# Kernel tuning notes

Hardware: AMD Instinct MI355X
Metric: run time of the kernel (lower is better)

The kernel has to match this reference:

```python
import jax, jax.numpy as jnp
import numpy as np
from jax import lax


def setup_inputs() -> dict:
    key = jax.random.key(0)
    ks = jax.random.split(key, 8)
    N, L, I, H = 256, 512, 512, 1024
    s_i = 1.0 / np.sqrt(H)
    x = jax.random.normal(ks[0], (N, L, I), dtype=jnp.float32)
    h = jnp.zeros((N, H), dtype=jnp.float32)
    # GRUCell params (torch layout: weight_ih [3H, I], weight_hh [3H, H], gate order r,z,n)
    W_ih = jax.random.uniform(ks[1], (3 * H, I), dtype=jnp.float32, minval=-s_i, maxval=s_i)
    b_ih = jax.random.uniform(ks[2], (3 * H,), dtype=jnp.float32, minval=-s_i, maxval=s_i)
    W_hh = jax.random.uniform(ks[3], (3 * H, H), dtype=jnp.float32, minval=-s_i, maxval=s_i)
    b_hh = jax.random.uniform(ks[4], (3 * H,), dtype=jnp.float32, minval=-s_i, maxval=s_i)
    # fc_out: Linear(H, I)
    W_out = jax.random.uniform(ks[5], (I, H), dtype=jnp.float32, minval=-s_i, maxval=s_i)
    b_out = jax.random.uniform(ks[6], (I,), dtype=jnp.float32, minval=-s_i, maxval=s_i)
    return {"x": x, "h": h, "W_ih": W_ih, "b_ih": b_ih, "W_hh": W_hh, "b_hh": b_hh,
            "W_out": W_out, "b_out": b_out}


def reference(x, h, W_ih, b_ih, W_hh, b_hh, W_out, b_out):
    # Many-to-one GRU: scan GRUCell over time, linear head on final hidden state.
    def step(h, xt):
        gi = xt @ W_ih.T + b_ih          # [N, 3H]
        gh = h @ W_hh.T + b_hh           # [N, 3H]
        i_r, i_z, i_n = jnp.split(gi, 3, axis=-1)
        h_r, h_z, h_n = jnp.split(gh, 3, axis=-1)
        r = jax.nn.sigmoid(i_r + h_r)
        z = jax.nn.sigmoid(i_z + h_z)
        n = jnp.tanh(i_n + r * h_n)
        h_new = (1.0 - z) * n + z * h
        return h_new, None

    xs = jnp.swapaxes(x, 0, 1)           # [L, N, I] for scan over time
    h_final, _ = lax.scan(step, h, xs)
    y = h_final @ W_out.T + b_out        # [N, I]
    return (y, h_final)
```

## Files before the change

kernel.cpp:

```cpp
#include <hip/hip_runtime.h>


typedef unsigned short u16;
typedef unsigned int   u32;
typedef __attribute__((ext_vector_type(4))) float f32x4;
typedef __attribute__((ext_vector_type(8))) short s16x8;

constexpr int NB   = 256;
constexpr int LSEQ = 512;
constexpr int ISZ  = 512;
constexpr int HSZ  = 1024;

constexpr int TILE_U16  = 48 * 1536;
constexpr int TILEBYTES = TILE_U16 * 2;
constexpr int LDS_TOTAL = TILEBYTES;

__device__ __forceinline__ u16 bf16_trunc(float f) {
    union { float f; unsigned u; } v; v.f = f;
    return (u16)(v.u >> 16);
}
__device__ __forceinline__ float bf16_up(u16 h) {
    union { float f; unsigned u; } v; v.u = ((unsigned)h) << 16;
    return v.f;
}
__device__ __forceinline__ u16 bf16_rtn(float f) {
    union { float f; unsigned u; } v; v.f = f;
    u32 u = v.u;
    u += 0x7FFFu + ((u >> 16) & 1u);
    return (u16)(u >> 16);
}

#define GLL16(g, l) __builtin_amdgcn_global_load_lds(                          \
    (const __attribute__((address_space(1))) u32*)(g),                         \
    (__attribute__((address_space(3))) u32*)(l), 16, 0, 0)

#define MFMA2(acc, a, b_h, b_l)                                              \
    acc = __builtin_amdgcn_mfma_f32_16x16x32_bf16(a, b_h, acc, 0, 0, 0);     \
    acc = __builtin_amdgcn_mfma_f32_16x16x32_bf16(a, b_l, acc, 0, 0, 0);

__global__ __launch_bounds__(256) void prep_kernel(
    const float* __restrict__ W_ih, const float* __restrict__ W_hh,
    const float* __restrict__ b_ih, const float* __restrict__ b_hh,
    const float* __restrict__ W_out,
    u16* __restrict__ Bhi, u16* __restrict__ Blo,
    float* __restrict__ Wt, float4* __restrict__ bias4)
{
    int idx = blockIdx.x * 256 + threadIdx.x;
    if (idx < 64 * TILE_U16) {
        int c   = idx / TILE_U16;
        int r1  = idx % TILE_U16;
        int kb  = r1 / 1536;
        int r2  = r1 % 1536;
        int p   = r2 / 512;
        int r3  = r2 % 512;
        int kg  = r3 >> 7;
        int col = (r3 >> 3) & 15;
        int e   = r3 & 7;
        int kloc = kg * 8 + e;
        int gcol = c * 16 + col;
        float w;
        if (kb < 16) w = W_ih[(p * HSZ + gcol) * ISZ + kb * 32 + kloc];
        else         w = W_hh[(p * HSZ + gcol) * HSZ + (kb - 16) * 32 + kloc];
        u16 hi = bf16_trunc(w);
        Bhi[idx] = hi;
        Blo[idx] = bf16_trunc(w - bf16_up(hi));
    }
    if (idx < HSZ * ISZ) {
        int i = idx % ISZ, k = idx / ISZ;
        Wt[idx] = W_out[i * HSZ + k];
    }
    if (idx < HSZ) {
        bias4[idx] = make_float4(b_ih[idx] + b_hh[idx],
                                 b_ih[HSZ + idx] + b_hh[HSZ + idx],
                                 b_ih[2 * HSZ + idx],
                                 b_hh[2 * HSZ + idx]);
    }
}

__global__ __launch_bounds__(256) void init_kernel(
    const float* __restrict__ x, const float* __restrict__ h_in,
    u16* __restrict__ xb0, float* __restrict__ hf0, u16* __restrict__ hb0)
{
    int idx = blockIdx.x * 256 + threadIdx.x;
    {
        int n = idx >> 9, k = idx & (ISZ - 1);
        xb0[idx] = bf16_rtn(x[(size_t)n * (LSEQ * ISZ) + k]);
    }
    #pragma unroll
    for (int q = 0; q < 2; ++q) {
        int e = idx * 2 + q;
        float v = h_in[e];
        hf0[e] = v;
        hb0[e] = bf16_rtn(v);
    }
}

__global__ __launch_bounds__(768, 1) void gru_step(
    const float* __restrict__ x, int t,
    const u16* __restrict__ Bhi, const u16* __restrict__ Blo,
    const float4* __restrict__ bias4,
    const u16* __restrict__ xb, u16* __restrict__ xb_n,
    const float* __restrict__ hf, const u16* __restrict__ hb,
    float* __restrict__ hf_n, u16* __restrict__ hb_n)
{
    extern __shared__ char lds[];

    const int tid  = threadIdx.x;
    const int lane = tid & 63;
    const int wv   = tid >> 6;
    const int raw  = blockIdx.x;
    const int c    = ((raw & 7) << 3) | ((raw >> 3) & 7);
    const int m    = raw >> 6;
    const int lr   = lane & 15;
    const int kg   = lane >> 4;
    const int fro  = kg * 256 + lr * 16;

    const char* tsrc = (const char*)Bhi + (size_t)c * TILEBYTES;

    #pragma unroll
    for (int i = 0; i < 12; ++i) {
        int seg = i * 12 + wv;
        GLL16(tsrc + seg * 1024 + lane * 16, lds + seg * 1024);
    }

    if (t + 1 < LSEQ && tid < 512) {
        int e = raw * 512 + tid;
        int n = e >> 9, k = e & (ISZ - 1);
        xb_n[e] = bf16_rtn(x[(size_t)n * (LSEQ * ISZ) + (size_t)(t + 1) * ISZ + k]);
    }

    __syncthreads();

    f32x4 acc[4][4];
    #pragma unroll
    for (int rt = 0; rt < 4; ++rt)
        #pragma unroll
        for (int s = 0; s < 4; ++s) acc[rt][s] = (f32x4){0.f, 0.f, 0.f, 0.f};

    const u16* blo = Blo + (size_t)c * TILE_U16;
    const bool isx = (wv < 4);

    #pragma unroll
    for (int j = 0; j < 4; ++j) {
        const int kbg = wv * 4 + j;
        const char* lp = lds + kbg * 3072 + fro;
        s16x8 bh0 = *(const s16x8*)lp;
        s16x8 bh1 = *(const s16x8*)(lp + 1024);
        s16x8 bh2 = *(const s16x8*)(lp + 2048);
        const u16* gp = blo + kbg * 1536 + kg * 128 + lr * 8;
        s16x8 bl0 = *(const s16x8*)gp;
        s16x8 bl1 = *(const s16x8*)(gp + 512);
        s16x8 bl2 = *(const s16x8*)(gp + 1024);

        #pragma unroll
        for (int rt = 0; rt < 4; ++rt) {
            const int row = m * 64 + rt * 16 + lr;
            s16x8 a;
            if (isx) a = *(const s16x8*)(xb + row * ISZ + kbg * 32 + kg * 8);
            else     a = *(const s16x8*)(hb + row * HSZ + (kbg - 16) * 32 + kg * 8);
            MFMA2(acc[rt][0], a, bh0, bl0)
            MFMA2(acc[rt][1], a, bh1, bl1)
            if (isx) { MFMA2(acc[rt][2], a, bh2, bl2) }
            else     { MFMA2(acc[rt][3], a, bh2, bl2) }
        }
    }

    float* scrf = (float*)lds;
    __syncthreads();
    if (wv >= 6) {
        float* sp = scrf + (wv - 6) * 4096 + lane * 4;
        #pragma unroll
        for (int rt = 0; rt < 4; ++rt)
            #pragma unroll
            for (int s = 0; s < 4; ++s)
                *(f32x4*)(sp + (rt * 4 + s) * 256) = acc[rt][s];
    }
    __syncthreads();
    if (wv < 6) {
        const float* sp = scrf + wv * 4096 + lane * 4;
        #pragma unroll
        for (int rt = 0; rt < 4; ++rt)
            #pragma unroll
            for (int s = 0; s < 4; ++s)
                acc[rt][s] += *(const f32x4*)(sp + (rt * 4 + s) * 256);
    }
    if (wv >= 3 && wv < 6) {
        float* sp = scrf + (wv + 3) * 4096 + lane * 4;
        #pragma unroll
        for (int rt = 0; rt < 4; ++rt)
            #pragma unroll
            for (int s = 0; s < 4; ++s)
                *(f32x4*)(sp + (rt * 4 + s) * 256) = acc[rt][s];
    }
    __syncthreads();
    if (wv < 3) {
        const float* sp = scrf + (wv + 6) * 4096 + lane * 4;
        float* wp = scrf + wv * 4096 + lane * 4;
        #pragma unroll
        for (int rt = 0; rt < 4; ++rt)
            #pragma unroll
            for (int s = 0; s < 4; ++s) {
                acc[rt][s] += *(const f32x4*)(sp + (rt * 4 + s) * 256);
                *(f32x4*)(wp + (rt * 4 + s) * 256) = acc[rt][s];
            }
    }
    __syncthreads();

    if (wv < 4) {
        const int rt = wv;
        f32x4 sr = {0,0,0,0}, sz = sr, sx = sr, sh = sr;
        #pragma unroll
        for (int sl = 0; sl < 3; ++sl) {
            const float* sp = scrf + sl * 4096 + lane * 4;
            sr += *(const f32x4*)(sp + (rt * 4 + 0) * 256);
            sz += *(const f32x4*)(sp + (rt * 4 + 1) * 256);
            sx += *(const f32x4*)(sp + (rt * 4 + 2) * 256);
            sh += *(const f32x4*)(sp + (rt * 4 + 3) * 256);
        }
        const int j = c * 16 + lr;
        const float4 b4 = bias4[j];
        #pragma unroll
        for (int i = 0; i < 4; ++i) {
            const int row = m * 64 + rt * 16 + kg * 4 + i;
            float rr  = 1.f / (1.f + __expf(-(sr[i] + b4.x)));
            float zz  = 1.f / (1.f + __expf(-(sz[i] + b4.y)));
            float pre = (sx[i] + b4.z) + rr * (sh[i] + b4.w);
            float e2  = __expf(2.f * pre);
            float ng  = 1.f - 2.f / (e2 + 1.f);
            float ho  = hf[row * HSZ + j];
            float hn  = (1.f - zz) * ng + zz * ho;
            hf_n[row * HSZ + j] = hn;
            hb_n[row * HSZ + j] = bf16_rtn(hn);
        }
    }
}

__global__ __launch_bounds__(256) void head_kernel(
    const float* __restrict__ hfin, const float* __restrict__ Wt,
    const float* __restrict__ b_out, float* __restrict__ out)
{
    __shared__ float hrow[HSZ];
    const int n = blockIdx.x;
    const int tid = threadIdx.x;
    for (int k = tid; k < HSZ; k += 256) {
        float v = hfin[n * HSZ + k];
        hrow[k] = v;
        out[NB * ISZ + n * HSZ + k] = v;
    }
    __syncthreads();
    for (int j = tid; j < ISZ; j += 256) {
        float acc = b_out[j];
        #pragma unroll 8
        for (int k = 0; k < HSZ; ++k)
            acc = fmaf(hrow[k], Wt[k * ISZ + j], acc);
        out[n * ISZ + j] = acc;
    }
}

extern "C" void kernel_launch(void* const* d_in, const int* in_sizes, int n_in,
                              void* d_out, int out_size, void* d_ws, size_t ws_size,
                              hipStream_t stream) {
    (void)in_sizes; (void)n_in; (void)out_size; (void)ws_size;
    const float* x     = (const float*)d_in[0];
    const float* h_in  = (const float*)d_in[1];
    const float* W_ih  = (const float*)d_in[2];
    const float* b_ih  = (const float*)d_in[3];
    const float* W_hh  = (const float*)d_in[4];
    const float* b_hh  = (const float*)d_in[5];
    const float* W_out = (const float*)d_in[6];
    const float* b_out = (const float*)d_in[7];
    float* out = (float*)d_out;

    char* ws = (char*)d_ws;
    size_t o = 0;
    u16*    Bhi   = (u16*)(ws + o);    o += (size_t)64 * TILEBYTES;
    u16*    Blo   = (u16*)(ws + o);    o += (size_t)64 * TILEBYTES;
    float*  Wt    = (float*)(ws + o);  o += (size_t)HSZ * ISZ * 4;
    float4* bias4 = (float4*)(ws + o); o += (size_t)HSZ * 16;
    float* hf[2]; u16 *hb[2], *xb[2];
    for (int b = 0; b < 2; ++b) { hf[b] = (float*)(ws + o); o += (size_t)NB * HSZ * 4; }
    for (int b = 0; b < 2; ++b) { hb[b] = (u16*)(ws + o);   o += (size_t)NB * HSZ * 2; }
    for (int b = 0; b < 2; ++b) { xb[b] = (u16*)(ws + o);   o += (size_t)NB * ISZ * 2; }

    prep_kernel<<<(64 * TILE_U16) / 256, 256, 0, stream>>>(
        W_ih, W_hh, b_ih, b_hh, W_out, Bhi, Blo, Wt, bias4);
    init_kernel<<<(NB * ISZ) / 256, 256, 0, stream>>>(
        x, h_in, xb[0], hf[0], hb[0]);

    for (int t = 0; t < LSEQ; ++t) {
        const int cur = t & 1, nxt = cur ^ 1;
        gru_step<<<256, 768, LDS_TOTAL, stream>>>(
            x, t, Bhi, Blo, bias4,
            xb[cur], xb[nxt],
            hf[cur], hb[cur],
            hf[nxt], hb[nxt]);
    }
    head_kernel<<<NB, 256, 0, stream>>>(hf[0], Wt, b_out, out);
}
```

Before: 6.747 ms.

## Replace per-timestep launches with persistent cooperative kernel and global atomic barriers

Turns the 512 per-step kernel launches into one cooperative persistent kernel with 256 blocks. Steps are synchronised through per-step atomic counters in global memory. Only the W_hh hi tile stays resident in LDS and the W_hh lo fragments are held in registers across steps. The input projection for step t+1 is computed right after each step, straight from fp32 x, so it overlaps the wait for the next barrier. This removes launch overhead and the repeated weight-tile reloads, at the cost of relaxed-atomic barrier correctness risk and higher register pressure with 512 threads and 2 blocks per CU.

```diff
diff --git a/kernel.cpp b/kernel.cpp
--- a/kernel.cpp
+++ b/kernel.cpp
@@ -1,8 +1,10 @@
 #include <hip/hip_runtime.h>
+#include <hip/hip_cooperative_groups.h>
 
 
 typedef unsigned short u16;
 typedef unsigned int   u32;
+typedef unsigned long long u64;
 typedef __attribute__((ext_vector_type(4))) float f32x4;
 typedef __attribute__((ext_vector_type(8))) short s16x8;
 
@@ -13,20 +15,18 @@
 
 constexpr int TILE_U16  = 48 * 1536;
 constexpr int TILEBYTES = TILE_U16 * 2;
-constexpr int LDS_TOTAL = TILEBYTES;
+constexpr int BH_LDS    = 96 * 1024;
+constexpr int LDS_TOTAL = BH_LDS + 32768;
 
 __device__ __forceinline__ u16 bf16_trunc(float f) {
-    union { float f; unsigned u; } v; v.f = f;
-    return (u16)(v.u >> 16);
+    union { float f; u32 u; } v; v.f = f; return (u16)(v.u >> 16);
 }
 __device__ __forceinline__ float bf16_up(u16 h) {
-    union { float f; unsigned u; } v; v.u = ((unsigned)h) << 16;
-    return v.f;
+    union { float f; u32 u; } v; v.u = ((u32)h) << 16; return v.f;
 }
 __device__ __forceinline__ u16 bf16_rtn(float f) {
-    union { float f; unsigned u; } v; v.f = f;
-    u32 u = v.u;
-    u += 0x7FFFu + ((u >> 16) & 1u);
+    union { float f; u32 u; } v; v.f = f;
+    u32 u = v.u; u += 0x7FFFu + ((u >> 16) & 1u);
     return (u16)(u >> 16);
 }
 
@@ -34,9 +34,7 @@
     (const __attribute__((address_space(1))) u32*)(g),                         \
     (__attribute__((address_space(3))) u32*)(l), 16, 0, 0)
 
-#define MFMA2(acc, a, b_h, b_l)                                              \
-    acc = __builtin_amdgcn_mfma_f32_16x16x32_bf16(a, b_h, acc, 0, 0, 0);     \
-    acc = __builtin_amdgcn_mfma_f32_16x16x32_bf16(a, b_l, acc, 0, 0, 0);
+#define MF(a, b, c) __builtin_amdgcn_mfma_f32_16x16x32_bf16(a, b, c, 0, 0, 0)
 
 __global__ __launch_bounds__(256) void prep_kernel(
     const float* __restrict__ W_ih, const float* __restrict__ W_hh,
@@ -78,58 +76,58 @@
 }
 
 __global__ __launch_bounds__(256) void init_kernel(
-    const float* __restrict__ x, const float* __restrict__ h_in,
-    u16* __restrict__ xb0, float* __restrict__ hf0, u16* __restrict__ hb0)
+    const float* __restrict__ h_in,
+    float* __restrict__ hf, u16* __restrict__ hb0, u32* __restrict__ bar)
 {
     int idx = blockIdx.x * 256 + threadIdx.x;
-    {
-        int n = idx >> 9, k = idx & (ISZ - 1);
-        xb0[idx] = bf16_rtn(x[(size_t)n * (LSEQ * ISZ) + k]);
-    }
-    #pragma unroll
-    for (int q = 0; q < 2; ++q) {
-        int e = idx * 2 + q;
-        float v = h_in[e];
-        hf0[e] = v;
-        hb0[e] = bf16_rtn(v);
-    }
-}
-
-__global__ __launch_bounds__(768, 1) void gru_step(
-    const float* __restrict__ x, int t,
+    float v = h_in[idx];
+    hf[idx]  = v;
+    hb0[idx] = bf16_rtn(v);
+    if (idx < LSEQ) bar[idx] = 0;
+}
+
+__global__ __launch_bounds__(512, 2) void gru_persistent(
+    const float* __restrict__ x,
     const u16* __restrict__ Bhi, const u16* __restrict__ Blo,
     const float4* __restrict__ bias4,
-    const u16* __restrict__ xb, u16* __restrict__ xb_n,
-    const float* __restrict__ hf, const u16* __restrict__ hb,
-    float* __restrict__ hf_n, u16* __restrict__ hb_n)
+    float* __restrict__ hf, u16* __restrict__ hb0, u16* __restrict__ hb1,
+    u32* __restrict__ bar)
 {
     extern __shared__ char lds[];
+    float* scr = (float*)(lds + BH_LDS);
 
     const int tid  = threadIdx.x;
     const int lane = tid & 63;
     const int wv   = tid >> 6;
+    const int lr   = lane & 15;
+    const int kg   = lane >> 4;
     const int raw  = blockIdx.x;
     const int c    = ((raw & 7) << 3) | ((raw >> 3) & 7);
     const int m    = raw >> 6;
-    const int lr   = lane & 15;
-    const int kg   = lane >> 4;
-    const int fro  = kg * 256 + lr * 16;
-
-    const char* tsrc = (const char*)Bhi + (size_t)c * TILEBYTES;
-
+    const int fro  = kg * 128 + lr * 8;
+    const int frob = fro * 2;
+
+    const u16* bhit = Bhi + (size_t)c * TILE_U16;
+    const u16* blot = Blo + (size_t)c * TILE_U16;
+
+    {
+        const char* src = (const char*)bhit + 16 * 3072;
+        #pragma unroll
+        for (int i = 0; i < 12; ++i) {
+            int seg = i * 8 + wv;
+            GLL16(src + seg * 1024 + lane * 16, lds + seg * 1024);
+        }
+    }
+
+    s16x8 BLr[4][3];
     #pragma unroll
-    for (int i = 0; i < 12; ++i) {
-        int seg = i * 12 + wv;
-        GLL16(tsrc + seg * 1024 + lane * 16, lds + seg * 1024);
-    }
-
-    if (t + 1 < LSEQ && tid < 512) {
-        int e = raw * 512 + tid;
-        int n = e >> 9, k = e & (ISZ - 1);
-        xb_n[e] = bf16_rtn(x[(size_t)n * (LSEQ * ISZ) + (size_t)(t + 1) * ISZ + k]);
-    }
-
-    __syncthreads();
+    for (int j = 0; j < 4; ++j) {
+        const int kb = 16 + wv * 4 + j;
+        #pragma unroll
+        for (int p = 0; p < 3; ++p)
+            BLr[j][p] = *(const s16x8*)(blot + kb * 1536 + p * 512 + fro);
+    }
+    const float4 b4 = bias4[c * 16 + lr];
 
     f32x4 acc[4][4];
     #pragma unroll
@@ -137,101 +135,175 @@
         #pragma unroll
         for (int s = 0; s < 4; ++s) acc[rt][s] = (f32x4){0.f, 0.f, 0.f, 0.f};
 
-    const u16* blo = Blo + (size_t)c * TILE_U16;
-    const bool isx = (wv < 4);
-
-    #pragma unroll
-    for (int j = 0; j < 4; ++j) {
-        const int kbg = wv * 4 + j;
-        const char* lp = lds + kbg * 3072 + fro;
-        s16x8 bh0 = *(const s16x8*)lp;
-        s16x8 bh1 = *(const s16x8*)(lp + 1024);
-        s16x8 bh2 = *(const s16x8*)(lp + 2048);
-        const u16* gp = blo + kbg * 1536 + kg * 128 + lr * 8;
-        s16x8 bl0 = *(const s16x8*)gp;
-        s16x8 bl1 = *(const s16x8*)(gp + 512);
-        s16x8 bl2 = *(const s16x8*)(gp + 1024);
-
-        #pragma unroll
-        for (int rt = 0; rt < 4; ++rt) {
-            const int row = m * 64 + rt * 16 + lr;
-            s16x8 a;
-            if (isx) a = *(const s16x8*)(xb + row * ISZ + kbg * 32 + kg * 8);
-            else     a = *(const s16x8*)(hb + row * HSZ + (kbg - 16) * 32 + kg * 8);
-            MFMA2(acc[rt][0], a, bh0, bl0)
-            MFMA2(acc[rt][1], a, bh1, bl1)
-            if (isx) { MFMA2(acc[rt][2], a, bh2, bl2) }
-            else     { MFMA2(acc[rt][3], a, bh2, bl2) }
-        }
-    }
-
-    float* scrf = (float*)lds;
-    __syncthreads();
-    if (wv >= 6) {
-        float* sp = scrf + (wv - 6) * 4096 + lane * 4;
+    auto xpart = [&](int tt) {
+        #pragma unroll
+        for (int jx = 0; jx < 2; ++jx) {
+            const int kb = wv * 2 + jx;
+            s16x8 xh[3], xl[3];
+            #pragma unroll
+            for (int p = 0; p < 3; ++p) {
+                xh[p] = *(const s16x8*)(bhit + kb * 1536 + p * 512 + fro);
+                xl[p] = *(const s16x8*)(blot + kb * 1536 + p * 512 + fro);
+            }
+            #pragma unroll
+            for (int rt = 0; rt < 4; ++rt) {
+                const int row = m * 64 + rt * 16 + lr;
+                const float* xp = x + ((size_t)row * LSEQ + tt) * ISZ + kb * 32 + kg * 8;
+                f32x4 a0 = *(const f32x4*)xp;
+                f32x4 a1 = *(const f32x4*)(xp + 4);
+                s16x8 a;
+                #pragma unroll
+                for (int e = 0; e < 4; ++e) {
+                    a[e]     = (short)bf16_rtn(a0[e]);
+                    a[e + 4] = (short)bf16_rtn(a1[e]);
+                }
+                acc[rt][0] = MF(a, xh[0], acc[rt][0]);
+                acc[rt][0] = MF(a, xl[0], acc[rt][0]);
+                acc[rt][1] = MF(a, xh[1], acc[rt][1]);
+                acc[rt][1] = MF(a, xl[1], acc[rt][1]);
+                acc[rt][2] = MF(a, xh[2], acc[rt][2]);
+                acc[rt][2] = MF(a, xl[2], acc[rt][2]);
+            }
+        }
+    };
+    xpart(0);
+
+    for (int t = 0; t < LSEQ; ++t) {
+        if (t > 0 && tid == 0) {
+            while (__hip_atomic_load(&bar[t - 1], __ATOMIC_RELAXED,
+                                     __HIP_MEMORY_SCOPE_AGENT) < 256u)
+                __builtin_amdgcn_s_sleep(2);
+        }
+        __syncthreads();
+
+        const u16* hbc = (t & 1) ? hb1 : hb0;
+        u16*       hbn = (t & 1) ? hb0 : hb1;
+
+        s16x8 a[4][4];
+        #pragma unroll
+        for (int j = 0; j < 4; ++j) {
+            const int khoff = (wv * 4 + j) * 32;
+            #pragma unroll
+            for (int rt = 0; rt < 4; ++rt) {
+                const int row = m * 64 + rt * 16 + lr;
+                u64* ap = (u64*)(hbc + (size_t)row * HSZ + khoff + kg * 8);
+                u64 w0 = __hip_atomic_load(ap,     __ATOMIC_RELAXED, __HIP_MEMORY_SCOPE_AGENT);
+                u64 w1 = __hip_atomic_load(ap + 1, __ATOMIC_RELAXED, __HIP_MEMORY_SCOPE_AGENT);
+                union { u64 q[2]; s16x8 v; } uu; uu.q[0] = w0; uu.q[1] = w1;
+                a[j][rt] = uu.v;
+            }
+        }
+        #pragma unroll
+        for (int j = 0; j < 4; ++j) {
+            const char* lp = lds + (wv * 4 + j) * 3072 + frob;
+            s16x8 bh0 = *(const s16x8*)lp;
+            s16x8 bh1 = *(const s16x8*)(lp + 1024);
+            s16x8 bh2 = *(const s16x8*)(lp + 2048);
+            #pragma unroll
+            for (int rt = 0; rt < 4; ++rt) {
+                acc[rt][0] = MF(a[j][rt], bh0, acc[rt][0]);
+                acc[rt][0] = MF(a[j][rt], BLr[j][0], acc[rt][0]);
+                acc[rt][1] = MF(a[j][rt], bh1, acc[rt][1]);
+                acc[rt][1] = MF(a[j][rt], BLr[j][1], acc[rt][1]);
+                acc[rt][3] = MF(a[j][rt], bh2, acc[rt][3]);
+                acc[rt][3] = MF(a[j][rt], BLr[j][2], acc[rt][3]);
+            }
+        }
+
+        __syncthreads();
+        #pragma unroll
+        for (int ph = 0; ph < 2; ++ph) {
+            if (wv >= 4) {
+                float* sp = scr + (wv - 4) * 2048 + lane * 4;
+                #pragma unroll
+                for (int rt = 0; rt < 4; ++rt)
+                    #pragma unroll
+                    for (int q = 0; q < 2; ++q)
+                        *(f32x4*)(sp + (rt * 2 + q) * 256) = acc[rt][ph * 2 + q];
+            }
+            __syncthreads();
+            if (wv < 4) {
+                const float* sp = scr + wv * 2048 + lane * 4;
+                #pragma unroll
+                for (int rt = 0; rt < 4; ++rt)
+                    #pragma unroll
+                    for (int q = 0; q < 2; ++q)
+                        acc[rt][ph * 2 + q] += *(const f32x4*)(sp + (rt * 2 + q) * 256);
+            }
+            __syncthreads();
+        }
+        if (wv == 2 || wv == 3) {
+            float* sp0 = scr + (wv - 2) * 2 * 2048 + lane * 4;
+            #pragma unroll
+            for (int rt = 0; rt < 4; ++rt)
+                #pragma unroll
+                for (int s = 0; s < 4; ++s)
+                    *(f32x4*)(sp0 + (s >> 1) * 2048 + (rt * 2 + (s & 1)) * 256) = acc[rt][s];
+        }
+        __syncthreads();
+        if (wv < 2) {
+            const float* sp0 = scr + wv * 2 * 2048 + lane * 4;
+            #pragma unroll
+            for (int rt = 0; rt < 4; ++rt)
+                #pragma unroll
+                for (int s = 0; s < 4; ++s)
+                    acc[rt][s] += *(const f32x4*)(sp0 + (s >> 1) * 2048 + (rt * 2 + (s & 1)) * 256);
+        }
+        __syncthreads();
+        if (wv == 0) {
+            float* sp = scr + lane * 4;
+            #pragma unroll
+            for (int rr = 0; rr < 2; ++rr)
+                #pragma unroll
+                for (int s = 0; s < 4; ++s)
+                    *(f32x4*)(sp + (rr * 4 + s) * 256) = acc[2 + rr][s];
+        } else if (wv == 1) {
+            float* sp = scr + 2048 + lane * 4;
+            #pragma unroll
+            for (int rr = 0; rr < 2; ++rr)
+                #pragma unroll
+                for (int s = 0; s < 4; ++s)
+                    *(f32x4*)(sp + (rr * 4 + s) * 256) = acc[rr][s];
+        }
+        __syncthreads();
+        if (wv < 2) {
+            const int rt0 = (wv == 0) ? 0 : 2;
+            const float* sp = scr + (1 - wv) * 2048 + lane * 4;
+            #pragma unroll
+            for (int rr = 0; rr < 2; ++rr)
+                #pragma unroll
+                for (int s = 0; s < 4; ++s)
+                    acc[rt0 + rr][s] += *(const f32x4*)(sp + (rr * 4 + s) * 256);
+            const int j = c * 16 + lr;
+            #pragma unroll
+            for (int rr = 0; rr < 2; ++rr) {
+                const int rt = rt0 + rr;
+                #pragma unroll
+                for (int i = 0; i < 4; ++i) {
+                    const int row = m * 64 + rt * 16 + kg * 4 + i;
+                    float r_ = 1.f / (1.f + __expf(-(acc[rt][0][i] + b4.x)));
+                    float z_ = 1.f / (1.f + __expf(-(acc[rt][1][i] + b4.y)));
+                    float pre = (acc[rt][2][i] + b4.z) + r_ * (acc[rt][3][i] + b4.w);
+                    float e2 = __expf(2.f * pre);
+                    float ng = 1.f - 2.f / (e2 + 1.f);
+                    float ho = hf[row * HSZ + j];
+                    float hn = (1.f - z_) * ng + z_ * ho;
+                    hf[row * HSZ + j] = hn;
+                    __hip_atomic_store(&hbn[row * HSZ + j], bf16_rtn(hn),
+                                       __ATOMIC_RELAXED, __HIP_MEMORY_SCOPE_AGENT);
+                }
+            }
+        }
+        __syncthreads();
+        if (tid == 0)
+            __hip_atomic_fetch_add(&bar[t], 1u, __ATOMIC_RELAXED,
+                                   __HIP_MEMORY_SCOPE_AGENT);
+
         #pragma unroll
         for (int rt = 0; rt < 4; ++rt)
             #pragma unroll
-            for (int s = 0; s < 4; ++s)
-                *(f32x4*)(sp + (rt * 4 + s) * 256) = acc[rt][s];
-    }
-    __syncthreads();
-    if (wv < 6) {
-        const float* sp = scrf + wv * 4096 + lane * 4;
-        #pragma unroll
-        for (int rt = 0; rt < 4; ++rt)
-            #pragma unroll
-            for (int s = 0; s < 4; ++s)
-                acc[rt][s] += *(const f32x4*)(sp + (rt * 4 + s) * 256);
-    }
-    if (wv >= 3 && wv < 6) {
-        float* sp = scrf + (wv + 3) * 4096 + lane * 4;
-        #pragma unroll
-        for (int rt = 0; rt < 4; ++rt)
-            #pragma unroll
-            for (int s = 0; s < 4; ++s)
-                *(f32x4*)(sp + (rt * 4 + s) * 256) = acc[rt][s];
-    }
-    __syncthreads();
-    if (wv < 3) {
-        const float* sp = scrf + (wv + 6) * 4096 + lane * 4;
-        float* wp = scrf + wv * 4096 + lane * 4;
-        #pragma unroll
-        for (int rt = 0; rt < 4; ++rt)
-            #pragma unroll
-            for (int s = 0; s < 4; ++s) {
-                acc[rt][s] += *(const f32x4*)(sp + (rt * 4 + s) * 256);
-                *(f32x4*)(wp + (rt * 4 + s) * 256) = acc[rt][s];
-            }
-    }
-    __syncthreads();
-
-    if (wv < 4) {
-        const int rt = wv;
-        f32x4 sr = {0,0,0,0}, sz = sr, sx = sr, sh = sr;
-        #pragma unroll
-        for (int sl = 0; sl < 3; ++sl) {
-            const float* sp = scrf + sl * 4096 + lane * 4;
-            sr += *(const f32x4*)(sp + (rt * 4 + 0) * 256);
-            sz += *(const f32x4*)(sp + (rt * 4 + 1) * 256);
-            sx += *(const f32x4*)(sp + (rt * 4 + 2) * 256);
-            sh += *(const f32x4*)(sp + (rt * 4 + 3) * 256);
-        }
-        const int j = c * 16 + lr;
-        const float4 b4 = bias4[j];
-        #pragma unroll
-        for (int i = 0; i < 4; ++i) {
-            const int row = m * 64 + rt * 16 + kg * 4 + i;
-            float rr  = 1.f / (1.f + __expf(-(sr[i] + b4.x)));
-            float zz  = 1.f / (1.f + __expf(-(sz[i] + b4.y)));
-            float pre = (sx[i] + b4.z) + rr * (sh[i] + b4.w);
-            float e2  = __expf(2.f * pre);
-            float ng  = 1.f - 2.f / (e2 + 1.f);
-            float ho  = hf[row * HSZ + j];
-            float hn  = (1.f - zz) * ng + zz * ho;
-            hf_n[row * HSZ + j] = hn;
-            hb_n[row * HSZ + j] = bf16_rtn(hn);
-        }
+            for (int s = 0; s < 4; ++s) acc[rt][s] = (f32x4){0.f, 0.f, 0.f, 0.f};
+        if (t + 1 < LSEQ) xpart(t + 1);
     }
 }
 
@@ -277,23 +349,29 @@
     u16*    Blo   = (u16*)(ws + o);    o += (size_t)64 * TILEBYTES;
     float*  Wt    = (float*)(ws + o);  o += (size_t)HSZ * ISZ * 4;
     float4* bias4 = (float4*)(ws + o); o += (size_t)HSZ * 16;
-    float* hf[2]; u16 *hb[2], *xb[2];
-    for (int b = 0; b < 2; ++b) { hf[b] = (float*)(ws + o); o += (size_t)NB * HSZ * 4; }
-    for (int b = 0; b < 2; ++b) { hb[b] = (u16*)(ws + o);   o += (size_t)NB * HSZ * 2; }
-    for (int b = 0; b < 2; ++b) { xb[b] = (u16*)(ws + o);   o += (size_t)NB * ISZ * 2; }
+    float*  hf    = (float*)(ws + o);  o += (size_t)NB * HSZ * 4;
+    u16*    hb0   = (u16*)(ws + o);    o += (size_t)NB * HSZ * 2;
+    u16*    hb1   = (u16*)(ws + o);    o += (size_t)NB * HSZ * 2;
+    u32*    bar   = (u32*)(ws + o);    o += (size_t)LSEQ * 4;
 
     prep_kernel<<<(64 * TILE_U16) / 256, 256, 0, stream>>>(
         W_ih, W_hh, b_ih, b_hh, W_out, Bhi, Blo, Wt, bias4);
-    init_kernel<<<(NB * ISZ) / 256, 256, 0, stream>>>(
-        x, h_in, xb[0], hf[0], hb[0]);
-
-    for (int t = 0; t < LSEQ; ++t) {
-        const int cur = t & 1, nxt = cur ^ 1;
-        gru_step<<<256, 768, LDS_TOTAL, stream>>>(
-            x, t, Bhi, Blo, bias4,
-            xb[cur], xb[nxt],
-            hf[cur], hb[cur],
-            hf[nxt], hb[nxt]);
-    }
-    head_kernel<<<NB, 256, 0, stream>>>(hf[0], Wt, b_out, out);
-}
+    init_kernel<<<(NB * HSZ) / 256, 256, 0, stream>>>(h_in, hf, hb0, bar);
+
+    {
+        const float* xp = x;
+        const u16* bhip = Bhi;
+        const u16* blop = Blo;
+        const float4* b4p = bias4;
+        float* hfp = hf;
+        u16* h0p = hb0;
+        u16* h1p = hb1;
+        u32* barp = bar;
+        void* args[] = {(void*)&xp, (void*)&bhip, (void*)&blop, (void*)&b4p,
+                        (void*)&hfp, (void*)&h0p, (void*)&h1p, (void*)&barp};
+        hipLaunchCooperativeKernel((void*)gru_persistent, dim3(256), dim3(512),
+                                   args, LDS_TOTAL, stream);
+    }
+
+    head_kernel<<<NB, 256, 0, stream>>>(hf, Wt, b_out, out);
+}
```

Measured after the change: 22.84 ms. +238.5%, slower.

## Drop LDS weight staging, use 8 waves with tree reduction and in-place hf

Applied to the files above, without the earlier changes.

The per-step kernel stops copying the bf16-hi weight tile into LDS and instead has every wave read both hi and lo weight fragments directly from global memory. The block shrinks from 12 to 8 waves, each covering 6 K-blocks, and the cross-wave reduction becomes a pairwise tree that ends in wave 0, which alone computes the gate math. The fp32 hidden state is updated in place, removing one buffer. The aim is to cut the LDS fill and barrier cost each step, at the price of more global/L2 traffic for weights and a serial epilogue on a single wave.

```diff
diff --git a/kernel.cpp b/kernel.cpp
--- a/kernel.cpp
+++ b/kernel.cpp
@@ -13,30 +13,21 @@
 
 constexpr int TILE_U16  = 48 * 1536;
 constexpr int TILEBYTES = TILE_U16 * 2;
-constexpr int LDS_TOTAL = TILEBYTES;
+constexpr int LDS_BYTES = 65536;
 
 __device__ __forceinline__ u16 bf16_trunc(float f) {
-    union { float f; unsigned u; } v; v.f = f;
-    return (u16)(v.u >> 16);
+    union { float f; u32 u; } v; v.f = f; return (u16)(v.u >> 16);
 }
 __device__ __forceinline__ float bf16_up(u16 h) {
-    union { float f; unsigned u; } v; v.u = ((unsigned)h) << 16;
-    return v.f;
+    union { float f; u32 u; } v; v.u = ((u32)h) << 16; return v.f;
 }
 __device__ __forceinline__ u16 bf16_rtn(float f) {
-    union { float f; unsigned u; } v; v.f = f;
-    u32 u = v.u;
-    u += 0x7FFFu + ((u >> 16) & 1u);
+    union { float f; u32 u; } v; v.f = f;
+    u32 u = v.u; u += 0x7FFFu + ((u >> 16) & 1u);
     return (u16)(u >> 16);
 }
 
-#define GLL16(g, l) __builtin_amdgcn_global_load_lds(                          \
-    (const __attribute__((address_space(1))) u32*)(g),                         \
-    (__attribute__((address_space(3))) u32*)(l), 16, 0, 0)
-
-#define MFMA2(acc, a, b_h, b_l)                                              \
-    acc = __builtin_amdgcn_mfma_f32_16x16x32_bf16(a, b_h, acc, 0, 0, 0);     \
-    acc = __builtin_amdgcn_mfma_f32_16x16x32_bf16(a, b_l, acc, 0, 0, 0);
+#define MF(a, b, c) __builtin_amdgcn_mfma_f32_16x16x32_bf16(a, b, c, 0, 0, 0)
 
 __global__ __launch_bounds__(256) void prep_kernel(
     const float* __restrict__ W_ih, const float* __restrict__ W_hh,
@@ -95,41 +86,34 @@
     }
 }
 
-__global__ __launch_bounds__(768, 1) void gru_step(
+__global__ __launch_bounds__(512, 1) void gru_step(
     const float* __restrict__ x, int t,
     const u16* __restrict__ Bhi, const u16* __restrict__ Blo,
     const float4* __restrict__ bias4,
     const u16* __restrict__ xb, u16* __restrict__ xb_n,
-    const float* __restrict__ hf, const u16* __restrict__ hb,
-    float* __restrict__ hf_n, u16* __restrict__ hb_n)
+    float* __restrict__ hf,
+    const u16* __restrict__ hb, u16* __restrict__ hb_n)
 {
-    extern __shared__ char lds[];
+    extern __shared__ float scr[];
 
     const int tid  = threadIdx.x;
     const int lane = tid & 63;
     const int wv   = tid >> 6;
+    const int lr   = lane & 15;
+    const int kg   = lane >> 4;
     const int raw  = blockIdx.x;
     const int c    = ((raw & 7) << 3) | ((raw >> 3) & 7);
     const int m    = raw >> 6;
-    const int lr   = lane & 15;
-    const int kg   = lane >> 4;
-    const int fro  = kg * 256 + lr * 16;
-
-    const char* tsrc = (const char*)Bhi + (size_t)c * TILEBYTES;
-
-    #pragma unroll
-    for (int i = 0; i < 12; ++i) {
-        int seg = i * 12 + wv;
-        GLL16(tsrc + seg * 1024 + lane * 16, lds + seg * 1024);
-    }
-
-    if (t + 1 < LSEQ && tid < 512) {
+    const int fro  = kg * 128 + lr * 8;
+
+    if (t + 1 < LSEQ) {
         int e = raw * 512 + tid;
         int n = e >> 9, k = e & (ISZ - 1);
         xb_n[e] = bf16_rtn(x[(size_t)n * (LSEQ * ISZ) + (size_t)(t + 1) * ISZ + k]);
     }
 
-    __syncthreads();
+    const u16* bhit = Bhi + (size_t)c * TILE_U16;
+    const u16* blot = Blo + (size_t)c * TILE_U16;
 
     f32x4 acc[4][4];
     #pragma unroll
@@ -137,38 +121,56 @@
         #pragma unroll
         for (int s = 0; s < 4; ++s) acc[rt][s] = (f32x4){0.f, 0.f, 0.f, 0.f};
 
-    const u16* blo = Blo + (size_t)c * TILE_U16;
-    const bool isx = (wv < 4);
-
-    #pragma unroll
-    for (int j = 0; j < 4; ++j) {
-        const int kbg = wv * 4 + j;
-        const char* lp = lds + kbg * 3072 + fro;
-        s16x8 bh0 = *(const s16x8*)lp;
-        s16x8 bh1 = *(const s16x8*)(lp + 1024);
-        s16x8 bh2 = *(const s16x8*)(lp + 2048);
-        const u16* gp = blo + kbg * 1536 + kg * 128 + lr * 8;
-        s16x8 bl0 = *(const s16x8*)gp;
-        s16x8 bl1 = *(const s16x8*)(gp + 512);
-        s16x8 bl2 = *(const s16x8*)(gp + 1024);
-
+    #pragma unroll 2
+    for (int j = 0; j < 6; ++j) {
+        const int kb = wv * 6 + j;
+        const u16* gh = bhit + kb * 1536 + fro;
+        const u16* gl = blot + kb * 1536 + fro;
+        s16x8 bh0 = *(const s16x8*)gh;
+        s16x8 bh1 = *(const s16x8*)(gh + 512);
+        s16x8 bh2 = *(const s16x8*)(gh + 1024);
+        s16x8 bl0 = *(const s16x8*)gl;
+        s16x8 bl1 = *(const s16x8*)(gl + 512);
+        s16x8 bl2 = *(const s16x8*)(gl + 1024);
+        const bool isx = (kb < 16);
+        s16x8 a[4];
+        if (isx) {
+            #pragma unroll
+            for (int rt = 0; rt < 4; ++rt) {
+                const int row = m * 64 + rt * 16 + lr;
+                a[rt] = *(const s16x8*)(xb + row * ISZ + kb * 32 + kg * 8);
+            }
+        } else {
+            #pragma unroll
+            for (int rt = 0; rt < 4; ++rt) {
+                const int row = m * 64 + rt * 16 + lr;
+                a[rt] = *(const s16x8*)(hb + row * HSZ + (kb - 16) * 32 + kg * 8);
+            }
+        }
         #pragma unroll
         for (int rt = 0; rt < 4; ++rt) {
-            const int row = m * 64 + rt * 16 + lr;
-            s16x8 a;
-            if (isx) a = *(const s16x8*)(xb + row * ISZ + kbg * 32 + kg * 8);
-            else     a = *(const s16x8*)(hb + row * HSZ + (kbg - 16) * 32 + kg * 8);
-            MFMA2(acc[rt][0], a, bh0, bl0)
-            MFMA2(acc[rt][1], a, bh1, bl1)
-            if (isx) { MFMA2(acc[rt][2], a, bh2, bl2) }
-            else     { MFMA2(acc[rt][3], a, bh2, bl2) }
+            acc[rt][0] = MF(a[rt], bh0, acc[rt][0]);
+            acc[rt][0] = MF(a[rt], bl0, acc[rt][0]);
+            acc[rt][1] = MF(a[rt], bh1, acc[rt][1]);
+            acc[rt][1] = MF(a[rt], bl1, acc[rt][1]);
         }
-    }
-
-    float* scrf = (float*)lds;
-    __syncthreads();
-    if (wv >= 6) {
-        float* sp = scrf + (wv - 6) * 4096 + lane * 4;
+        if (isx) {
+            #pragma unroll
+            for (int rt = 0; rt < 4; ++rt) {
+                acc[rt][2] = MF(a[rt], bh2, acc[rt][2]);
+                acc[rt][2] = MF(a[rt], bl2, acc[rt][2]);
+            }
+        } else {
+            #pragma unroll
+            for (int rt = 0; rt < 4; ++rt) {
+                acc[rt][3] = MF(a[rt], bh2, acc[rt][3]);
+                acc[rt][3] = MF(a[rt], bl2, acc[rt][3]);
+            }
+        }
+    }
+
+    if (wv >= 4) {
+        float* sp = scr + (wv - 4) * 4096 + lane * 4;
         #pragma unroll
         for (int rt = 0; rt < 4; ++rt)
             #pragma unroll
@@ -176,16 +178,17 @@
                 *(f32x4*)(sp + (rt * 4 + s) * 256) = acc[rt][s];
     }
     __syncthreads();
-    if (wv < 6) {
-        const float* sp = scrf + wv * 4096 + lane * 4;
+    if (wv < 4) {
+        const float* sp = scr + wv * 4096 + lane * 4;
         #pragma unroll
         for (int rt = 0; rt < 4; ++rt)
             #pragma unroll
             for (int s = 0; s < 4; ++s)
                 acc[rt][s] += *(const f32x4*)(sp + (rt * 4 + s) * 256);
     }
-    if (wv >= 3 && wv < 6) {
-        float* sp = scrf + (wv + 3) * 4096 + lane * 4;
+    __syncthreads();
+    if (wv == 2 || wv == 3) {
+        float* sp = scr + (wv - 2) * 4096 + lane * 4;
         #pragma unroll
         for (int rt = 0; rt < 4; ++rt)
             #pragma unroll
@@ -193,44 +196,48 @@
                 *(f32x4*)(sp + (rt * 4 + s) * 256) = acc[rt][s];
     }
     __syncthreads();
-    if (wv < 3) {
-        const float* sp = scrf + (wv + 6) * 4096 + lane * 4;
-        float* wp = scrf + wv * 4096 + lane * 4;
-        #pragma unroll
-        for (int rt = 0; rt < 4; ++rt)
-            #pragma unroll
-            for (int s = 0; s < 4; ++s) {
+    if (wv < 2) {
+        const float* sp = scr + wv * 4096 + lane * 4;
+        #pragma unroll
+        for (int rt = 0; rt < 4; ++rt)
+            #pragma unroll
+            for (int s = 0; s < 4; ++s)
                 acc[rt][s] += *(const f32x4*)(sp + (rt * 4 + s) * 256);
-                *(f32x4*)(wp + (rt * 4 + s) * 256) = acc[rt][s];
-            }
-    }
-    __syncthreads();
-
-    if (wv < 4) {
-        const int rt = wv;
-        f32x4 sr = {0,0,0,0}, sz = sr, sx = sr, sh = sr;
-        #pragma unroll
-        for (int sl = 0; sl < 3; ++sl) {
-            const float* sp = scrf + sl * 4096 + lane * 4;
-            sr += *(const f32x4*)(sp + (rt * 4 + 0) * 256);
-            sz += *(const f32x4*)(sp + (rt * 4 + 1) * 256);
-            sx += *(const f32x4*)(sp + (rt * 4 + 2) * 256);
-            sh += *(const f32x4*)(sp + (rt * 4 + 3) * 256);
-        }
+    }
+    __syncthreads();
+    if (wv == 1) {
+        float* sp = scr + lane * 4;
+        #pragma unroll
+        for (int rt = 0; rt < 4; ++rt)
+            #pragma unroll
+            for (int s = 0; s < 4; ++s)
+                *(f32x4*)(sp + (rt * 4 + s) * 256) = acc[rt][s];
+    }
+    __syncthreads();
+    if (wv == 0) {
+        const float* sp = scr + lane * 4;
+        #pragma unroll
+        for (int rt = 0; rt < 4; ++rt)
+            #pragma unroll
+            for (int s = 0; s < 4; ++s)
+                acc[rt][s] += *(const f32x4*)(sp + (rt * 4 + s) * 256);
         const int j = c * 16 + lr;
         const float4 b4 = bias4[j];
         #pragma unroll
-        for (int i = 0; i < 4; ++i) {
-            const int row = m * 64 + rt * 16 + kg * 4 + i;
-            float rr  = 1.f / (1.f + __expf(-(sr[i] + b4.x)));
-            float zz  = 1.f / (1.f + __expf(-(sz[i] + b4.y)));
-            float pre = (sx[i] + b4.z) + rr * (sh[i] + b4.w);
-            float e2  = __expf(2.f * pre);
-            float ng  = 1.f - 2.f / (e2 + 1.f);
-            float ho  = hf[row * HSZ + j];
-            float hn  = (1.f - zz) * ng + zz * ho;
-            hf_n[row * HSZ + j] = hn;
-            hb_n[row * HSZ + j] = bf16_rtn(hn);
+        for (int rt = 0; rt < 4; ++rt) {
+            #pragma unroll
+            for (int i = 0; i < 4; ++i) {
+                const int row = m * 64 + rt * 16 + kg * 4 + i;
+                float r_ = 1.f / (1.f + __expf(-(acc[rt][0][i] + b4.x)));
+                float z_ = 1.f / (1.f + __expf(-(acc[rt][1][i] + b4.y)));
+                float pre = (acc[rt][2][i] + b4.z) + r_ * (acc[rt][3][i] + b4.w);
+                float e2 = __expf(2.f * pre);
+                float ng = 1.f - 2.f / (e2 + 1.f);
+                float ho = hf[row * HSZ + j];
+                float hn = (1.f - z_) * ng + z_ * ho;
+                hf[row * HSZ + j] = hn;
+                hb_n[row * HSZ + j] = bf16_rtn(hn);
+            }
         }
     }
 }
@@ -277,23 +284,22 @@
     u16*    Blo   = (u16*)(ws + o);    o += (size_t)64 * TILEBYTES;
     float*  Wt    = (float*)(ws + o);  o += (size_t)HSZ * ISZ * 4;
     float4* bias4 = (float4*)(ws + o); o += (size_t)HSZ * 16;
-    float* hf[2]; u16 *hb[2], *xb[2];
-    for (int b = 0; b < 2; ++b) { hf[b] = (float*)(ws + o); o += (size_t)NB * HSZ * 4; }
-    for (int b = 0; b < 2; ++b) { hb[b] = (u16*)(ws + o);   o += (size_t)NB * HSZ * 2; }
-    for (int b = 0; b < 2; ++b) { xb[b] = (u16*)(ws + o);   o += (size_t)NB * ISZ * 2; }
+    float*  hf    = (float*)(ws + o);  o += (size_t)NB * HSZ * 4;
+    u16* hb[2]; u16* xb[2];
+    for (int b = 0; b < 2; ++b) { hb[b] = (u16*)(ws + o); o += (size_t)NB * HSZ * 2; }
+    for (int b = 0; b < 2; ++b) { xb[b] = (u16*)(ws + o); o += (size_t)NB * ISZ * 2; }
 
     prep_kernel<<<(64 * TILE_U16) / 256, 256, 0, stream>>>(
         W_ih, W_hh, b_ih, b_hh, W_out, Bhi, Blo, Wt, bias4);
     init_kernel<<<(NB * ISZ) / 256, 256, 0, stream>>>(
-        x, h_in, xb[0], hf[0], hb[0]);
+        x, h_in, xb[0], hf, hb[0]);
 
     for (int t = 0; t < LSEQ; ++t) {
         const int cur = t & 1, nxt = cur ^ 1;
-        gru_step<<<256, 768, LDS_TOTAL, stream>>>(
+        gru_step<<<256, 512, LDS_BYTES, stream>>>(
             x, t, Bhi, Blo, bias4,
             xb[cur], xb[nxt],
-            hf[cur], hb[cur],
-            hf[nxt], hb[nxt]);
-    }
-    head_kernel<<<NB, 256, 0, stream>>>(hf[0], Wt, b_out, out);
-}
+            hf, hb[cur], hb[nxt]);
+    }
+    head_kernel<<<NB, 256, 0, stream>>>(hf, Wt, b_out, out);
+}
```

Result: slower. 7.019 ms (+4.0%).
